# Performance work log

Measured on AMD Instinct MI355X. Metric: run time of the kernel, lower is better.

The kernel has to match this reference:

```python
import jax, jax.numpy as jnp
import numpy as np
from jax import lax

N_FFT = 1024
N_FREQ = N_FFT // 2 + 1  # 513
BATCH = 32
SAMPLES = 480000
HOP = 256


def setup_inputs() -> dict:
    key = jax.random.key(0)
    kx, kwin = jax.random.split(key)
    x = jax.random.normal(kx, (BATCH, 1, SAMPLES), dtype=jnp.float32)
    n = jnp.arange(N_FFT, dtype=jnp.float32)
    # standard rfft angular frequencies: w_k = 2*pi*k / N
    w = 2.0 * jnp.pi * jnp.arange(N_FREQ, dtype=jnp.float32) / N_FFT
    # Hann window (periodic), as typically used for STFT
    window = 0.5 - 0.5 * jnp.cos(2.0 * jnp.pi * jnp.arange(N_FFT, dtype=jnp.float32) / N_FFT)
    return {"x": x, "n": n, "w": w, "window": window, "hop_size": HOP, "power": 1}


def _create_dft_matrices(n, w, window):
    # temp[f, t] = w_f * n_t
    temp = w[:, None] * n[None, :]              # [n_freq, n_fft]
    Fr = jnp.cos(temp)
    Fi = -jnp.sin(temp)
    if window is not None:
        Fr = window * Fr
        Fi = window * Fi
    # conv1d weights: [out_ch=n_freq, in_ch=1, kernel=n_fft]
    return Fr[:, None, :], Fi[:, None, :]


def reference(x, n, w, window, hop_size, power):
    DFTr, DFTi = _create_dft_matrices(n, w, window)
    dn = ("NCH", "OIH", "NCH")
    real_x = lax.conv_general_dilated(x, DFTr, (hop_size,), "VALID", dimension_numbers=dn)
    imag_x = lax.conv_general_dilated(x, DFTi, (hop_size,), "VALID", dimension_numbers=dn)
    S = real_x ** 2 + imag_x ** 2              # [B, n_freq, n_frames]
    if not power:
        S = jnp.sqrt(S)
    return S
```

## Files before the change

### kernel.cpp

```cpp
#include <hip/hip_runtime.h>
#include <hip/hip_bf16.h>
#include <stdint.h>
#include <math.h>


#define NFFT     1024
#define NFREQ    513
#define BATCH    32
#define SAMPLES  480000
#define SAMPH    240000
#define HOPH     128
#define NFRAMES  1872
#define NCOLS    (BATCH * NFRAMES)
#define BN       256
#define MBLKS    4
#define NBLKS    (NCOLS / BN)
#define KTILES   16
#define NWG      (MBLKS * NBLKS)

#define XH_BYTES  ((size_t)BATCH * SAMPLES)
#define AWS_BYTES ((size_t)MBLKS * KTILES * 128 * 64)

#define XMAX   6.5f
#define SCALE_X (127.0f / XMAX)
#define DEQ    (XMAX / 16129.0f)
#define DEQ2   (DEQ * DEQ)

#define QX_BLOCKS 1875
#define BA_BLOCKS 2048
#define PREP_BLOCKS (QX_BLOCKS + BA_BLOCKS)

typedef __attribute__((ext_vector_type(4)))  int i32x4;
typedef __attribute__((ext_vector_type(16))) int i32x16;

#define SLOTM(r) ((((r) >> 1) & 3) ^ (((r) >> 3) & 1))

__global__ __launch_bounds__(256) void k_prep(const float* __restrict__ x,
                                              const float* __restrict__ narr,
                                              const float* __restrict__ w,
                                              const float* __restrict__ window,
                                              signed char* __restrict__ xe,
                                              signed char* __restrict__ xo,
                                              signed char* __restrict__ Aws) {
  const int bid = blockIdx.x;
  const int tid = threadIdx.x;
  if (bid < QX_BLOCKS) {
    size_t i = (size_t)bid * 256 + tid;
    const float4* x4 = (const float4*)x;
    union { signed char c[16]; uint4 v; } pe, po;
    #pragma unroll
    for (int j = 0; j < 8; ++j) {
      float4 a = x4[i * 8 + j];
      float qe = fminf(127.f, fmaxf(-127.f, a.x * SCALE_X));
      float qo = fminf(127.f, fmaxf(-127.f, a.y * SCALE_X));
      float qe2 = fminf(127.f, fmaxf(-127.f, a.z * SCALE_X));
      float qo2 = fminf(127.f, fmaxf(-127.f, a.w * SCALE_X));
      pe.c[j * 2]     = (signed char)__float2int_rn(qe);
      po.c[j * 2]     = (signed char)__float2int_rn(qo);
      pe.c[j * 2 + 1] = (signed char)__float2int_rn(qe2);
      po.c[j * 2 + 1] = (signed char)__float2int_rn(qo2);
    }
    ((uint4*)xe)[i] = pe.v;
    ((uint4*)xo)[i] = po.v;
  } else {
    uint32_t E = (uint32_t)(bid - QX_BLOCKS) * 256 + tid;
    uint32_t e    = E & 15;
    uint32_t s    = (E >> 4) & 3;
    uint32_t r    = (E >> 6) & 127;
    uint32_t kt   = (E >> 13) & 15;
    uint32_t mblk = E >> 17;
    uint32_t er = mblk * 128 + r;
    uint32_t j  = (kt & 7) * 64 + ((s ^ SLOTM(r)) << 4) + e;
    uint32_t odd = (kt >> 3) & 1;
    uint32_t widx = (er == 1) ? 512u : (er & ~1u);
    float ang = w[widx] * narr[j];
    float sn, cs;
    sincosf(ang, &sn, &cs);
    float base = ((er & 1) && (er != 1)) ? -sn : cs;
    float val = 127.f * window[2 * j + odd] * base;
    Aws[E] = (signed char)__float2int_rn(val);
  }
}

#define GL2LDS(g, l) __builtin_amdgcn_global_load_lds( \
    (const __attribute__((address_space(1))) uint32_t*)(g), \
    (__attribute__((address_space(3))) uint32_t*)(l), 16, 0, 0)

#define WAITV1_BAR() asm volatile("s_waitcnt vmcnt(1)\ns_barrier" ::: "memory")
#define WAIT0_BAR()  asm volatile("s_waitcnt vmcnt(0)\ns_barrier" ::: "memory")
#define BAR()        asm volatile("s_barrier" ::: "memory")


#define STAGE_A(kt) do { const int P_ = (kt) & 1;                               \
  GL2LDS(Aws + (((size_t)mblk * KTILES + (kt)) * 512 + tid) * 16,               \
         &lds[P_ * 8192 + tid * 16]); } while (0)

#define STAGE_B(kt) do { const int P_ = (kt) & 1;                               \
  const signed char* bb_ = ((kt) < 8) ? xe : xo;                                \
  _Pragma("unroll") for (int h_ = 0; h_ < 2; ++h_) {                            \
    int ci_ = h_ * 512 + tid;                                                   \
    GL2LDS(bb_ + bsrc[h_] + ((kt) & 7) * 64,                                    \
           &lds[16384 + P_ * 16384 + ci_ * 16]); } } while (0)

#define READ_A(P)                                                               \
  _Pragma("unroll") for (int mt_ = 0; mt_ < 2; ++mt_)                           \
  _Pragma("unroll") for (int ks_ = 0; ks_ < 2; ++ks_) {                         \
    int r_ = wr * 64 + mt_ * 32 + lr;                                           \
    int sl_ = (ks_ * 2 + hi) ^ SLOTM(r_);                                       \
    a[mt_][ks_] = *(const i32x4*)&lds[(P) * 8192 + (r_ * 4 + sl_) * 16];        \
  }

#define READ_B(nt, P)                                                           \
  _Pragma("unroll") for (int ks_ = 0; ks_ < 2; ++ks_) {                         \
    int c_ = wc * 64 + (nt) * 32 + lr;                                          \
    int sl_ = (ks_ * 2 + hi) ^ SLOTM(c_);                                       \
    bfr[nt][ks_] = *(const i32x4*)&lds[16384 + (P) * 16384 + (c_ * 4 + sl_) * 16]; \
  }

#define MFMA_CL(ACC, nt) do {                                                   \
  __builtin_amdgcn_s_setprio(1);                                                \
  _Pragma("unroll") for (int ks_ = 0; ks_ < 2; ++ks_)                           \
  _Pragma("unroll") for (int mt_ = 0; mt_ < 2; ++mt_)                           \
    ACC[mt_][nt] = __builtin_amdgcn_mfma_i32_32x32x32_i8(                       \
        a[mt_][ks_], bfr[nt][ks_], ACC[mt_][nt], 0, 0, 0);                      \
  __builtin_amdgcn_s_setprio(0);                                                \
  } while (0)

#define KTBODY(kt, ACC) do {                                                    \
    const int P_k = (kt) & 1;                                                   \
    if ((kt) == KTILES - 1) WAIT0_BAR(); else WAITV1_BAR();                     \
    READ_A(P_k);                                                                \
    READ_B(0, P_k);                                                             \
    if ((kt) + 1 < KTILES) STAGE_B((kt) + 1);                                   \
    MFMA_CL(ACC, 0);                                                            \
    BAR();                                                                      \
    READ_B(1, P_k);                                                             \
    if ((kt) + 2 < KTILES) STAGE_A((kt) + 2);                                   \
    MFMA_CL(ACC, 1);                                                            \
  } while (0)

__global__ __launch_bounds__(512, 2) void k_stft(const signed char* __restrict__ xe,
                                                 const signed char* __restrict__ xo,
                                                 const signed char* __restrict__ Aws,
                                                 float* __restrict__ out) {
  __shared__ signed char lds[49152];
  const int tid  = threadIdx.x;
  const int lane = tid & 63;
  const int wid  = tid >> 6;
  const int wr = wid >> 2;
  const int wc = wid & 3;
  const int lr = lane & 31;
  const int hi = lane >> 5;

  const int bx = blockIdx.x;
  const int v = (bx & 7) * 117 + (bx >> 3);
  const int nblk = v >> 2;
  const int mblk = v & 3;

  size_t bsrc[2];
  #pragma unroll
  for (int h = 0; h < 2; ++h) {
    int col = h * 128 + (tid >> 2);
    int kc = (tid & 3) ^ SLOTM(col);
    int jcol = nblk * BN + col;
    int b = jcol / NFRAMES;
    int tf = jcol - b * NFRAMES;
    bsrc[h] = (size_t)b * SAMPH + (size_t)tf * HOPH + kc * 16;
  }

  i32x16 accE[2][2], accO[2][2];
  #pragma unroll
  for (int i = 0; i < 2; ++i)
    #pragma unroll
    for (int j = 0; j < 2; ++j)
      #pragma unroll
      for (int e = 0; e < 16; ++e) { accE[i][j][e] = 0; accO[i][j][e] = 0; }

  i32x4 a[2][2];
  i32x4 bfr[2][2];

  STAGE_A(0);
  STAGE_B(0);
  STAGE_A(1);

  #pragma unroll 2
  for (int kt = 0; kt < 8; ++kt)  KTBODY(kt, accE);
  #pragma unroll 2
  for (int kt = 8; kt < 16; ++kt) KTBODY(kt, accO);

  const int fbase = mblk * 64 + wr * 32;
  float ctab[16], stab[16];
  #pragma unroll
  for (int mt = 0; mt < 2; ++mt)
    #pragma unroll
    for (int aa = 0; aa < 4; ++aa)
      #pragma unroll
      for (int q = 0; q < 2; ++q) {
        int idx = mt * 8 + aa * 2 + q;
        float fq = (float)(fbase + mt * 16 + aa * 4 + 2 * hi + q);
        sincosf(fq * (float)(M_PI / 512.0), &stab[idx], &ctab[idx]);
      }
  const int colb = nblk * BN + wc * 64;
  #pragma unroll
  for (int nt = 0; nt < 2; ++nt) {
    const int col = colb + nt * 32 + lr;
    const int bo = col / NFRAMES;
    const int tf = col - bo * NFRAMES;
    float* op = out + (size_t)bo * (NFREQ * NFRAMES) + tf;
    #pragma unroll
    for (int mt = 0; mt < 2; ++mt) {
      i32x16 vE = accE[mt][nt];
      i32x16 vO = accO[mt][nt];
      #pragma unroll
      for (int aa = 0; aa < 4; ++aa)
        #pragma unroll
        for (int q = 0; q < 2; ++q) {
          const int fq = fbase + mt * 16 + aa * 4 + 2 * hi + q;
          float Ere = (float)vE[aa * 4 + 2 * q];
          float Eim = (float)vE[aa * 4 + 2 * q + 1];
          float Ore = (float)vO[aa * 4 + 2 * q];
          float Oim = (float)vO[aa * 4 + 2 * q + 1];
          if (fq == 0) {
            float sp = Ere + Ore, sm = Ere - Ore;
            op[0]                          = DEQ2 * sp * sp;
            op[(size_t)512 * NFRAMES]      = DEQ2 * sm * sm;
            op[(size_t)256 * NFRAMES]      = DEQ2 * (Eim * Eim + Oim * Oim);
          } else {
            const int idx = mt * 8 + aa * 2 + q;
            float ct = ctab[idx], st = stab[idx];
            float Pre = ct * Ore + st * Oim;
            float Pim = ct * Oim - st * Ore;
            float ar = Ere + Pre, ai = Eim + Pim;
            float br = Ere - Pre, bi = Eim - Pim;
            op[(size_t)fq * NFRAMES]         = DEQ2 * (ar * ar + ai * ai);
            op[(size_t)(512 - fq) * NFRAMES] = DEQ2 * (br * br + bi * bi);
          }
        }
    }
  }
}

extern "C" void kernel_launch(void* const* d_in, const int* in_sizes, int n_in,
                              void* d_out, int out_size, void* d_ws, size_t ws_size,
                              hipStream_t stream) {
  const float* x      = (const float*)d_in[0];
  const float* narr   = (const float*)d_in[1];
  const float* w      = (const float*)d_in[2];
  const float* window = (const float*)d_in[3];
  float* out = (float*)d_out;

  signed char* xe  = (signed char*)d_ws;
  signed char* xo  = xe + (size_t)BATCH * SAMPH;
  signed char* Aws = xo + (size_t)BATCH * SAMPH;
  if (ws_size < XH_BYTES + AWS_BYTES) return;

  k_prep<<<PREP_BLOCKS, 256, 0, stream>>>(x, narr, w, window, xe, xo, Aws);
  k_stft<<<NWG, 512, 0, stream>>>(xe, xo, Aws, out);
}
```

Baseline: 72.40 us.

## Stage contiguous per-batch sample streams in LDS and shrink column tile

Blocks now cover 128 frames within one batch instead of 256 flattened columns. Each block loads the contiguous even/odd sample stream for its frames into LDS once, and all K tiles read overlapping frame windows from it, exploiting the hop overlap rather than re-gathering per frame. The A matrix is ring-buffered four tiles deep, the per-iteration pipeline is restructured, occupancy is raised to 4 blocks, and the twiddle table is replaced by inline sincos. The cost is larger LDS per block (66 KB), which may not fit four blocks per CU, padding waste on the last tile of each batch, and lgkm barriers every iteration.

After: 78.59 us. 8.5% more time.

```diff
diff --git a/kernel.cpp b/kernel.cpp
--- a/kernel.cpp
+++ b/kernel.cpp
@@ -11,12 +11,11 @@
 #define SAMPH    240000
 #define HOPH     128
 #define NFRAMES  1872
-#define NCOLS    (BATCH * NFRAMES)
-#define BN       256
+#define BN       128
+#define NBPB     15
 #define MBLKS    4
-#define NBLKS    (NCOLS / BN)
 #define KTILES   16
-#define NWG      (MBLKS * NBLKS)
+#define NWG      (BATCH * NBPB * MBLKS)
 
 #define XH_BYTES  ((size_t)BATCH * SAMPLES)
 #define AWS_BYTES ((size_t)MBLKS * KTILES * 128 * 64)
@@ -51,8 +50,8 @@
     #pragma unroll
     for (int j = 0; j < 8; ++j) {
       float4 a = x4[i * 8 + j];
-      float qe = fminf(127.f, fmaxf(-127.f, a.x * SCALE_X));
-      float qo = fminf(127.f, fmaxf(-127.f, a.y * SCALE_X));
+      float qe  = fminf(127.f, fmaxf(-127.f, a.x * SCALE_X));
+      float qo  = fminf(127.f, fmaxf(-127.f, a.y * SCALE_X));
       float qe2 = fminf(127.f, fmaxf(-127.f, a.z * SCALE_X));
       float qo2 = fminf(127.f, fmaxf(-127.f, a.w * SCALE_X));
       pe.c[j * 2]     = (signed char)__float2int_rn(qe);
@@ -86,64 +85,67 @@
     (const __attribute__((address_space(1))) uint32_t*)(g), \
     (__attribute__((address_space(3))) uint32_t*)(l), 16, 0, 0)
 
-#define WAITV1_BAR() asm volatile("s_waitcnt vmcnt(1)\ns_barrier" ::: "memory")
+#define WAITV2_BAR() asm volatile("s_waitcnt vmcnt(2)\ns_barrier" ::: "memory")
 #define WAIT0_BAR()  asm volatile("s_waitcnt vmcnt(0)\ns_barrier" ::: "memory")
-#define BAR()        asm volatile("s_barrier" ::: "memory")
-
-
-#define STAGE_A(kt) do { const int P_ = (kt) & 1;                               \
-  GL2LDS(Aws + (((size_t)mblk * KTILES + (kt)) * 512 + tid) * 16,               \
-         &lds[P_ * 8192 + tid * 16]); } while (0)
-
-#define STAGE_B(kt) do { const int P_ = (kt) & 1;                               \
-  const signed char* bb_ = ((kt) < 8) ? xe : xo;                                \
-  _Pragma("unroll") for (int h_ = 0; h_ < 2; ++h_) {                            \
-    int ci_ = h_ * 512 + tid;                                                   \
-    GL2LDS(bb_ + bsrc[h_] + ((kt) & 7) * 64,                                    \
-           &lds[16384 + P_ * 16384 + ci_ * 16]); } } while (0)
-
-#define READ_A(P)                                                               \
+#define LGKM0_BAR()  asm volatile("s_waitcnt lgkmcnt(0)\ns_barrier" ::: "memory")
+
+#define SE 0
+#define SO 17408
+#define AR 34816
+
+#define STAGE_STREAM(src, bl) do {                                              \
+  _Pragma("unroll") for (int p_ = 0; p_ < 2; ++p_) {                            \
+    int q_ = p_ * 512 + tid;                                                    \
+    GL2LDS((src) + ((q_ ^ ((q_ >> 3) & 7)) << 4), &lds[(bl) + q_ * 16]);        \
+  }                                                                             \
+  if (tid < 64) {                                                               \
+    int q_ = 1024 + tid;                                                        \
+    GL2LDS((src) + ((q_ ^ ((q_ >> 3) & 7)) << 4), &lds[(bl) + q_ * 16]);        \
+  }                                                                             \
+} while (0)
+
+#define STAGE_A(kt) GL2LDS(Aws + (((size_t)mblk * KTILES + (kt)) * 512 + tid) * 16, \
+                           &lds[AR + ((kt) & 3) * 8192 + tid * 16])
+
+#define READ_A2(dst, kt)                                                        \
   _Pragma("unroll") for (int mt_ = 0; mt_ < 2; ++mt_)                           \
   _Pragma("unroll") for (int ks_ = 0; ks_ < 2; ++ks_) {                         \
     int r_ = wr * 64 + mt_ * 32 + lr;                                           \
     int sl_ = (ks_ * 2 + hi) ^ SLOTM(r_);                                       \
-    a[mt_][ks_] = *(const i32x4*)&lds[(P) * 8192 + (r_ * 4 + sl_) * 16];        \
-  }
-
-#define READ_B(nt, P)                                                           \
+    dst[mt_][ks_] = *(const i32x4*)&lds[AR + ((kt) & 3) * 8192 + (r_ * 4 + sl_) * 16]; \
+  }
+
+#define READ_B2(dst, ktm7, SB)                                                  \
   _Pragma("unroll") for (int ks_ = 0; ks_ < 2; ++ks_) {                         \
-    int c_ = wc * 64 + (nt) * 32 + lr;                                          \
-    int sl_ = (ks_ * 2 + hi) ^ SLOTM(c_);                                       \
-    bfr[nt][ks_] = *(const i32x4*)&lds[16384 + (P) * 16384 + (c_ * 4 + sl_) * 16]; \
-  }
-
-#define MFMA_CL(ACC, nt) do {                                                   \
+    int cp_ = fl * 8 + (ktm7) * 4 + 2 * ks_ + hi;                               \
+    dst[ks_] = *(const i32x4*)&lds[(SB) + ((cp_ ^ ((cp_ >> 3) & 7)) << 4)];     \
+  }
+
+#define MFMA2(ACC, A_, B_) do {                                                 \
   __builtin_amdgcn_s_setprio(1);                                                \
   _Pragma("unroll") for (int ks_ = 0; ks_ < 2; ++ks_)                           \
   _Pragma("unroll") for (int mt_ = 0; mt_ < 2; ++mt_)                           \
-    ACC[mt_][nt] = __builtin_amdgcn_mfma_i32_32x32x32_i8(                       \
-        a[mt_][ks_], bfr[nt][ks_], ACC[mt_][nt], 0, 0, 0);                      \
+    ACC[mt_] = __builtin_amdgcn_mfma_i32_32x32x32_i8(                           \
+        A_[mt_][ks_], B_[ks_], ACC[mt_], 0, 0, 0);                              \
   __builtin_amdgcn_s_setprio(0);                                                \
   } while (0)
 
-#define KTBODY(kt, ACC) do {                                                    \
-    const int P_k = (kt) & 1;                                                   \
-    if ((kt) == KTILES - 1) WAIT0_BAR(); else WAITV1_BAR();                     \
-    READ_A(P_k);                                                                \
-    READ_B(0, P_k);                                                             \
-    if ((kt) + 1 < KTILES) STAGE_B((kt) + 1);                                   \
-    MFMA_CL(ACC, 0);                                                            \
-    BAR();                                                                      \
-    READ_B(1, P_k);                                                             \
-    if ((kt) + 2 < KTILES) STAGE_A((kt) + 2);                                   \
-    MFMA_CL(ACC, 1);                                                            \
+#define ITER(i, ACC, SB) do {                                                   \
+    if ((i) == 7) WAIT0_BAR(); else WAITV2_BAR();                               \
+    i32x4 a0[2][2], a1[2][2], b0[2], b1[2];                                     \
+    READ_A2(a0, 2 * (i));     READ_B2(b0, (2 * (i)) & 7, SB);                   \
+    READ_A2(a1, 2 * (i) + 1); READ_B2(b1, (2 * (i) + 1) & 7, SB);               \
+    MFMA2(ACC, a0, b0);                                                         \
+    MFMA2(ACC, a1, b1);                                                         \
+    LGKM0_BAR();                                                                \
+    if ((i) < 6) { STAGE_A(2 * (i) + 4); STAGE_A(2 * (i) + 5); }                \
   } while (0)
 
-__global__ __launch_bounds__(512, 2) void k_stft(const signed char* __restrict__ xe,
+__global__ __launch_bounds__(512, 4) void k_stft(const signed char* __restrict__ xe,
                                                  const signed char* __restrict__ xo,
                                                  const signed char* __restrict__ Aws,
                                                  float* __restrict__ out) {
-  __shared__ signed char lds[49152];
+  __shared__ __align__(16) signed char lds[67584];
   const int tid  = threadIdx.x;
   const int lane = tid & 63;
   const int wid  = tid >> 6;
@@ -151,66 +153,40 @@
   const int wc = wid & 3;
   const int lr = lane & 31;
   const int hi = lane >> 5;
+  const int fl = wc * 32 + lr;
 
   const int bx = blockIdx.x;
-  const int v = (bx & 7) * 117 + (bx >> 3);
-  const int nblk = v >> 2;
+  const int v = (bx & 7) * 240 + (bx >> 3);
   const int mblk = v & 3;
-
-  size_t bsrc[2];
-  #pragma unroll
-  for (int h = 0; h < 2; ++h) {
-    int col = h * 128 + (tid >> 2);
-    int kc = (tid & 3) ^ SLOTM(col);
-    int jcol = nblk * BN + col;
-    int b = jcol / NFRAMES;
-    int tf = jcol - b * NFRAMES;
-    bsrc[h] = (size_t)b * SAMPH + (size_t)tf * HOPH + kc * 16;
-  }
-
-  i32x16 accE[2][2], accO[2][2];
+  const int nb = v >> 2;
+  const int b  = nb / NBPB;
+  const int f0 = (nb - b * NBPB) * BN;
+
+  const signed char* se_src = xe + (size_t)b * SAMPH + (size_t)f0 * HOPH;
+  const signed char* so_src = xo + (size_t)b * SAMPH + (size_t)f0 * HOPH;
+
+  i32x16 accE[2], accO[2];
   #pragma unroll
   for (int i = 0; i < 2; ++i)
     #pragma unroll
-    for (int j = 0; j < 2; ++j)
-      #pragma unroll
-      for (int e = 0; e < 16; ++e) { accE[i][j][e] = 0; accO[i][j][e] = 0; }
-
-  i32x4 a[2][2];
-  i32x4 bfr[2][2];
-
-  STAGE_A(0);
-  STAGE_B(0);
-  STAGE_A(1);
-
-  #pragma unroll 2
-  for (int kt = 0; kt < 8; ++kt)  KTBODY(kt, accE);
-  #pragma unroll 2
-  for (int kt = 8; kt < 16; ++kt) KTBODY(kt, accO);
+    for (int e = 0; e < 16; ++e) { accE[i][e] = 0; accO[i][e] = 0; }
+
+  STAGE_STREAM(se_src, SE);
+  STAGE_STREAM(so_src, SO);
+  STAGE_A(0); STAGE_A(1); STAGE_A(2); STAGE_A(3);
+  WAIT0_BAR();
+
+  ITER(0, accE, SE); ITER(1, accE, SE); ITER(2, accE, SE); ITER(3, accE, SE);
+  ITER(4, accO, SO); ITER(5, accO, SO); ITER(6, accO, SO); ITER(7, accO, SO);
 
   const int fbase = mblk * 64 + wr * 32;
-  float ctab[16], stab[16];
-  #pragma unroll
-  for (int mt = 0; mt < 2; ++mt)
-    #pragma unroll
-    for (int aa = 0; aa < 4; ++aa)
-      #pragma unroll
-      for (int q = 0; q < 2; ++q) {
-        int idx = mt * 8 + aa * 2 + q;
-        float fq = (float)(fbase + mt * 16 + aa * 4 + 2 * hi + q);
-        sincosf(fq * (float)(M_PI / 512.0), &stab[idx], &ctab[idx]);
-      }
-  const int colb = nblk * BN + wc * 64;
-  #pragma unroll
-  for (int nt = 0; nt < 2; ++nt) {
-    const int col = colb + nt * 32 + lr;
-    const int bo = col / NFRAMES;
-    const int tf = col - bo * NFRAMES;
-    float* op = out + (size_t)bo * (NFREQ * NFRAMES) + tf;
+  const int tfi = f0 + fl;
+  if (tfi < NFRAMES) {
+    float* op = out + (size_t)b * ((size_t)NFREQ * NFRAMES) + tfi;
     #pragma unroll
     for (int mt = 0; mt < 2; ++mt) {
-      i32x16 vE = accE[mt][nt];
-      i32x16 vO = accO[mt][nt];
+      i32x16 vE = accE[mt];
+      i32x16 vO = accO[mt];
       #pragma unroll
       for (int aa = 0; aa < 4; ++aa)
         #pragma unroll
@@ -222,12 +198,12 @@
           float Oim = (float)vO[aa * 4 + 2 * q + 1];
           if (fq == 0) {
             float sp = Ere + Ore, sm = Ere - Ore;
-            op[0]                          = DEQ2 * sp * sp;
-            op[(size_t)512 * NFRAMES]      = DEQ2 * sm * sm;
-            op[(size_t)256 * NFRAMES]      = DEQ2 * (Eim * Eim + Oim * Oim);
+            op[0]                     = DEQ2 * sp * sp;
+            op[(size_t)512 * NFRAMES] = DEQ2 * sm * sm;
+            op[(size_t)256 * NFRAMES] = DEQ2 * (Eim * Eim + Oim * Oim);
           } else {
-            const int idx = mt * 8 + aa * 2 + q;
-            float ct = ctab[idx], st = stab[idx];
+            float st, ct;
+            sincosf((float)fq * (float)(M_PI / 512.0), &st, &ct);
             float Pre = ct * Ore + st * Oim;
             float Pim = ct * Oim - st * Ore;
             float ar = Ere + Pre, ai = Eim + Pim;
```
